# Kernel optimization log

Hardware: AMD Instinct MI355X
Metric: run time of the kernel (lower is better)

Reference implementation:

```python
import jax, jax.numpy as jnp
import numpy as np

N, D1, D2, B = 8, 2048, 1024, 512
D = D1 * D2
MAXBW = 3
NUM_PART = 5          # num_possible_partitions
TEMP = 0.01           # TEMPERATURE used in df_lt
DENOS = (3.0, 5.0, 17.0)  # 2^2-1, 2^2+1, 2^4+1


def ste_floor(x):
    # straight-through floor: forward floor, backward identity
    return x + jax.lax.stop_gradient(jnp.floor(x) - x)


def segmented_mean(piece, scheme, msp):
    """Replicates the inner python scan over sorted rows.
    piece:  (N, D) sorted residual errors
    scheme: (N-1, D) rounded split decisions (0/1), per column
    msp:    (N-1, D) soft split probabilities (grad factors), per column
    Returns (N, D): each row gets grad_ * (segment mean) of its segment.
    """
    n = piece.shape[0]
    buf = jnp.zeros_like(piece[0])
    cnt = jnp.zeros_like(piece[0])
    g = jnp.ones_like(piece[0])
    reset = jnp.zeros(piece.shape[1], dtype=bool)
    vlist, blist = [], []
    for i in range(n):
        buf = jnp.where(reset, piece[i], buf + piece[i])
        cnt = jnp.where(reset, 1.0, cnt + 1.0)
        g = jnp.where(reset, 1.0, g)
        if i == n - 1:
            vlist.append(g * (buf / cnt))
            blist.append(jnp.ones_like(reset))
        else:
            b = scheme[i] > 0.5
            vlist.append(jnp.where(b, g * msp[i], 0.0) * (buf / cnt))
            blist.append(b)
            g = jnp.where(b, g, g * (1.0 - msp[i]))
            reset = b
    # broadcast each segment-end value back to all rows of its segment
    out = vlist[-1]
    outs = [out]
    for i in range(n - 2, -1, -1):
        out = jnp.where(blist[i], vlist[i], out)
        outs.append(out)
    return jnp.stack(outs[::-1], axis=0)


def residual_quant(U, vsum, s, thr):
    """One residual quantization level (the update_partition=True branch)."""
    res = U - vsum                                   # (N, D)
    idx_maps = jnp.argsort(res, axis=0)              # torch.sort ascending, dim=0
    sorted_err = jnp.take_along_axis(res, idx_maps, axis=0)
    delta = sorted_err[1:] - sorted_err[:-1]         # (N-1, D), >= 0
    delta = delta / jnp.max(delta)
    msp = jax.nn.sigmoid((delta - thr) / TEMP)       # mean_split_point (N-1, D)
    rs = jnp.round(msp)                              # round_split, 0/1

    nm1 = N - 1
    P = 2 ** nm1  # all possible split-column patterns (torch.unique over dim=1)
    weights = (2 ** jnp.arange(nm1 - 1, -1, -1)).astype(jnp.int32)  # row 0 = MSB (lexicographic)
    code = jnp.sum(rs.astype(jnp.int32) * weights[:, None], axis=0)  # (D,)
    counts = jnp.zeros((P,), jnp.int32).at[code].add(1)
    present = counts > 0
    # torch.unique sorts patterns lexicographically -> rank = #present codes below
    rank_of_code = jnp.cumsum(present.astype(jnp.int32)) - present.astype(jnp.int32)
    order = jnp.argsort(-counts)                     # codes by count descending
    top_codes = order[:NUM_PART]
    top_ranks = rank_of_code[top_codes]              # s_indices[:NUM_PART]
    # binary patterns for every possible code
    patterns = ((jnp.arange(P)[:, None] >> jnp.arange(nm1 - 1, -1, -1)[None, :]) & 1).astype(jnp.float32)  # (P, N-1)
    inter = patterns @ patterns[top_codes].T         # (P, NUM_PART)
    sel = jnp.argmax(inter, axis=1)
    reassigned = top_ranks[sel]                      # (P,)
    is_top = jnp.any(rank_of_code[:, None] == top_ranks[None, :], axis=1)
    final_rank = jnp.where(is_top, rank_of_code, reassigned)  # (P,)
    c_rank = final_rank[code]                        # clustered_indices, (D,)

    # NOTE: original indexes round_split / mean_split_point columns BY the
    # unique-cluster index value s_idx (a quirk of the source); replicate it.
    scheme_used = rs[:, c_rank]                      # (N-1, D)
    msp_used = msp[:, c_rank]                        # (N-1, D)

    inner = segmented_mean(sorted_err, scheme_used, msp_used)  # (N, D)
    # einsum('cb,cba->ab', inner, one_hot(idx_maps)) == unsort along dim 0
    inv = jnp.argsort(idx_maps, axis=0)
    grouped = jnp.take_along_axis(inner, inv, axis=0)
    return s * ste_floor(grouped / s)


def setup_inputs():
    key = jax.random.key(0)
    k1, k2 = jax.random.split(key)
    x = jax.random.normal(k1, (B, N, D1), dtype=jnp.float32)
    # kaiming_normal_ on (N, D): std = sqrt(2 / fan_in), fan_in = D
    U = jax.random.normal(k2, (N, D), dtype=jnp.float32) * np.float32(np.sqrt(2.0 / D))
    thres_mean = jnp.full((D2,), -1.3, dtype=jnp.float32)
    return {"x": x, "U": U, "thres_mean": thres_mean}


def reference(x, U, thres_mean):
    beta = jnp.max(U)
    alpha = jnp.min(U)
    s = (beta - alpha) / DENOS[0]
    vsum = s * ste_floor(U / s)                      # base quantization level
    thr = jax.nn.sigmoid(jnp.repeat(thres_mean, D1))  # thres_mean.repeat_interleave(D1)
    for deno in DENOS[1:MAXBW]:
        s = s / deno
        vsum = vsum + residual_quant(U, vsum, s, thr)
    w = vsum.reshape(N, D1, D2)
    return jnp.einsum('bnd,ndl->bnl', x, w)
```

## Files before the change

### kernel.cpp

```cpp
#include <hip/hip_runtime.h>
#include <hip/hip_bf16.h>
#include <math.h>

#define NROW 8
#define DT   2097152
#define DD1  2048
#define DD2  1024
#define BATCH 512
#define NBLK4 2048


typedef __attribute__((ext_vector_type(8))) short short8;
typedef __attribute__((ext_vector_type(4))) float f32x4;

__device__ __forceinline__ unsigned fenc(float f){
  unsigned u = __float_as_uint(f);
  return (u & 0x80000000u) ? ~u : (u | 0x80000000u);
}
__device__ __forceinline__ float fdec(unsigned k){
  return (k & 0x80000000u) ? __uint_as_float(k ^ 0x80000000u) : __uint_as_float(~k);
}
__device__ __forceinline__ float sigmoid_ref(float z){
  #pragma clang fp contract(off)
  return 1.0f / (1.0f + expf(-z));
}
__device__ __forceinline__ unsigned short f2bf(float f){
  __hip_bfloat16 h = __float2bfloat16(f);
  return *reinterpret_cast<unsigned short*>(&h);
}
__device__ __forceinline__ float base1(float u, float s1, float inv_s1){
  #pragma clang fp contract(off)
  return s1 * floorf(u * inv_s1);
}
__device__ __forceinline__ void async16(const unsigned short* g, unsigned short* l){
  __builtin_amdgcn_global_load_lds((const __attribute__((address_space(1))) unsigned int*)g,
                                   (__attribute__((address_space(3))) unsigned int*)l, 16, 0, 0);
}

#define CSWAPV(a,b) { float _lo=fminf(a,b), _hi=fmaxf(a,b); a=_lo; b=_hi; }
__device__ __forceinline__ void sort8v(float v[8]){
  CSWAPV(v[0],v[1]) CSWAPV(v[2],v[3]) CSWAPV(v[4],v[5]) CSWAPV(v[6],v[7])
  CSWAPV(v[0],v[2]) CSWAPV(v[1],v[3]) CSWAPV(v[4],v[6]) CSWAPV(v[5],v[7])
  CSWAPV(v[1],v[2]) CSWAPV(v[5],v[6])
  CSWAPV(v[0],v[4]) CSWAPV(v[1],v[5]) CSWAPV(v[2],v[6]) CSWAPV(v[3],v[7])
  CSWAPV(v[2],v[4]) CSWAPV(v[3],v[5])
  CSWAPV(v[1],v[2]) CSWAPV(v[3],v[4]) CSWAPV(v[5],v[6])
}
__device__ __forceinline__ void cswapkv(float&av,int&ai,float&bv,int&bi){
  bool sw = (av > bv) || ((av == bv) && (ai > bi));
  float nav = sw ? bv : av; float nbv = sw ? av : bv;
  int   nai = sw ? bi : ai; int   nbi = sw ? ai : bi;
  av = nav; bv = nbv; ai = nai; bi = nbi;
}
#define CSWAPK(i,j) cswapkv(v[i],ix[i],v[j],ix[j]);
__device__ __forceinline__ void sort8kv(float v[8], int ix[8]){
  CSWAPK(0,1) CSWAPK(2,3) CSWAPK(4,5) CSWAPK(6,7)
  CSWAPK(0,2) CSWAPK(1,3) CSWAPK(4,6) CSWAPK(5,7)
  CSWAPK(1,2) CSWAPK(5,6)
  CSWAPK(0,4) CSWAPK(1,5) CSWAPK(2,6) CSWAPK(3,7)
  CSWAPK(2,4) CSWAPK(3,5)
  CSWAPK(1,2) CSWAPK(3,4) CSWAPK(5,6)
}

__global__ void k_init(unsigned* __restrict__ meta){
  int t = threadIdx.x;
  if (t == 0){ meta[0] = 0u; meta[1] = 0xFFFFFFFFu; meta[2] = 0u; meta[3] = 0u; }
  if (t < 128){ meta[4+t] = 0u; meta[132+t] = 0u; }
}

__global__ __launch_bounds__(256) void k_minmax(const float* __restrict__ U, unsigned* __restrict__ meta){
  __shared__ unsigned smx[256], smn[256];
  int t = threadIdx.x;
  size_t i = (size_t)blockIdx.x*256 + t;
  size_t stride = (size_t)gridDim.x*256;
  const float4* U4 = (const float4*)U;
  float mx = -INFINITY, mn = INFINITY;
  for (; i < (size_t)NROW*DT/4; i += stride){
    float4 v = U4[i];
    mx = fmaxf(fmaxf(mx,v.x), fmaxf(v.y, fmaxf(v.z,v.w)));
    mn = fminf(fminf(mn,v.x), fminf(v.y, fminf(v.z,v.w)));
  }
  smx[t] = fenc(mx); smn[t] = fenc(mn);
  __syncthreads();
  for (int o = 128; o > 0; o >>= 1){
    if (t < o){ smx[t] = max(smx[t], smx[t+o]); smn[t] = min(smn[t], smn[t+o]); }
    __syncthreads();
  }
  if (t == 0){ atomicMax(&meta[0], smx[0]); atomicMin(&meta[1], smn[0]); }
}

__global__ __launch_bounds__(256) void k_passA2(const float* __restrict__ U, unsigned* __restrict__ meta){
  #pragma clang fp contract(off)
  __shared__ unsigned sred[256];
  int t = threadIdx.x;
  int d0 = (blockIdx.x*256 + t)*4;
  float beta = fdec(meta[0]), alpha = fdec(meta[1]);
  float s1 = (beta - alpha) / 3.0f;
  float inv_s1 = 1.0f / s1;
  float4 u[8];
  #pragma unroll
  for (int i = 0; i < 8; ++i) u[i] = *(const float4*)(U + (size_t)i*DT + d0);
  unsigned dmax = 0u;
  #pragma unroll
  for (int c = 0; c < 4; ++c){
    float res[8];
    #pragma unroll
    for (int i = 0; i < 8; ++i){
      float uv = ((const float*)&u[i])[c];
      res[i] = uv - base1(uv, s1, inv_s1);
    }
    sort8v(res);
    float m = 0.0f;
    #pragma unroll
    for (int i = 0; i < 7; ++i) m = fmaxf(m, res[i+1] - res[i]);
    dmax = max(dmax, __float_as_uint(m));
  }
  sred[t] = dmax;
  __syncthreads();
  for (int o = 128; o > 0; o >>= 1){
    if (t < o) sred[t] = max(sred[t], sred[t+o]);
    __syncthreads();
  }
  if (t == 0) atomicMax(&meta[2], sred[0]);
}

template<int LEVEL>
__global__ __launch_bounds__(256) void k_passB(const float* __restrict__ U, const float* __restrict__ vsum,
                                               const float* __restrict__ thres_mean,
                                               unsigned char* __restrict__ code, unsigned* __restrict__ meta){
  #pragma clang fp contract(off)
  __shared__ int hist[128];
  int t = threadIdx.x;
  if (t < 128) hist[t] = 0;
  __syncthreads();
  int d0 = (blockIdx.x*256 + t)*4;
  float beta = fdec(meta[0]), alpha = fdec(meta[1]);
  float s1 = (beta - alpha) / 3.0f;
  float inv_s1 = 1.0f / s1;
  float gmax = __uint_as_float(meta[(LEVEL==2)?2:3]);
  float inv_gmax = 1.0f / gmax;
  float4 u[8], b[8];
  #pragma unroll
  for (int i = 0; i < 8; ++i){
    u[i] = *(const float4*)(U + (size_t)i*DT + d0);
    if (LEVEL == 2){
      float4 bb;
      bb.x = base1(u[i].x, s1, inv_s1); bb.y = base1(u[i].y, s1, inv_s1);
      bb.z = base1(u[i].z, s1, inv_s1); bb.w = base1(u[i].w, s1, inv_s1);
      b[i] = bb;
    } else {
      b[i] = *(const float4*)(vsum + (size_t)i*DT + d0);
    }
  }
  float thr = sigmoid_ref(thres_mean[d0 >> 11]);
  uchar4 cods;
  unsigned char* cp = (unsigned char*)&cods;
  #pragma unroll
  for (int c = 0; c < 4; ++c){
    float res[8];
    #pragma unroll
    for (int i = 0; i < 8; ++i) res[i] = ((const float*)&u[i])[c] - ((const float*)&b[i])[c];
    sort8v(res);
    int cd = 0;
    #pragma unroll
    for (int i = 0; i < 7; ++i){
      float dn = (res[i+1] - res[i]) * inv_gmax;
      int bit = (dn > thr) ? 1 : 0;
      cd = (cd << 1) | bit;
    }
    cp[c] = (unsigned char)cd;
    atomicAdd(&hist[cd], 1);
  }
  *(uchar4*)(code + d0) = cods;
  __syncthreads();
  if (t < 128 && hist[t] > 0) atomicAdd((int*)&meta[((LEVEL==2)?4:132) + t], hist[t]);
}

template<int LEVEL>
__global__ void k_small(const float* __restrict__ U, const float* __restrict__ vsum,
                        const float* __restrict__ thres_mean, unsigned* __restrict__ meta){
  #pragma clang fp contract(off)
  __shared__ int cs[128], rk[128], redk[128];
  __shared__ int top_code[5], top_rank[5];
  __shared__ int w0cnt;
  int c = threadIdx.x;
  cs[c] = (int)meta[((LEVEL==2)?4:132) + c];
  bool present = cs[c] > 0;
  unsigned long long bm = __ballot(present);
  int lane = c & 63;
  int r = (int)__popcll(bm & ((1ull << lane) - 1ull));
  if (c == 63) w0cnt = (int)__popcll(bm);
  __syncthreads();
  if (c >= 64) r += w0cnt;
  rk[c] = r;
  __syncthreads();
  for (int k = 0; k < 5; ++k){
    redk[c] = (cs[c] << 7) | (127 - c);
    __syncthreads();
    for (int o = 64; o > 0; o >>= 1){
      if (c < o) redk[c] = max(redk[c], redk[c+o]);
      __syncthreads();
    }
    if (c == 0){
      int best = 127 - (redk[0] & 127);
      top_code[k] = best; top_rank[k] = rk[best];
      cs[best] = -1;
    }
    __syncthreads();
  }
  int besti = -1, sel = 0;
  #pragma unroll
  for (int j = 0; j < 5; ++j){
    int inter = __popc(c & top_code[j]);
    if (inter > besti){ besti = inter; sel = j; }
  }
  bool is_top = false;
  #pragma unroll
  for (int j = 0; j < 5; ++j) is_top = is_top || (rk[c] == top_rank[j]);
  int fr = is_top ? rk[c] : top_rank[sel];
  ((int*)meta)[260 + c] = fr;
  float beta = fdec(meta[0]), alpha = fdec(meta[1]);
  float s1 = (beta - alpha) / 3.0f;
  float inv_s1 = 1.0f / s1;
  float gmax = __uint_as_float(meta[(LEVEL==2)?2:3]);
  float res[8];
  #pragma unroll
  for (int i = 0; i < 8; ++i){
    size_t off = (size_t)i*DT + c;
    float u = U[off];
    float b = (LEVEL==2) ? base1(u, s1, inv_s1) : vsum[off];
    res[i] = u - b;
  }
  sort8v(res);
  float thr = sigmoid_ref(thres_mean[c >> 11]);
  unsigned bits = 0;
  float* msp_tab = (float*)&meta[388];
  #pragma unroll
  for (int i = 0; i < 7; ++i){
    float dn  = (res[i+1] - res[i]) / gmax;
    float z   = (dn - thr) / 0.01f;
    float msp = sigmoid_ref(z);
    msp_tab[c*7 + i] = msp;
    bits |= ((unsigned)(int)rintf(msp)) << i;
  }
  meta[1284 + c] = bits;
}

template<int LEVEL>
__global__ __launch_bounds__(256) void k_passD(const float* __restrict__ U, float* __restrict__ vsum,
                                               const unsigned char* __restrict__ code,
                                               unsigned* __restrict__ meta){
  #pragma clang fp contract(off)
  __shared__ float q_lds[32*256];
  __shared__ int fr_s[128];
  __shared__ unsigned bits_s[128];
  __shared__ float msp_s[128*7];
  __shared__ unsigned sred[256];
  int t = threadIdx.x;
  if (t < 128){ fr_s[t] = ((int*)meta)[260 + t]; bits_s[t] = meta[1284 + t]; }
  for (int i = t; i < 128*7; i += 256) msp_s[i] = ((float*)&meta[388])[i];
  __syncthreads();
  int d0 = (blockIdx.x*256 + t)*4;
  float beta = fdec(meta[0]), alpha = fdec(meta[1]);
  float s1 = (beta - alpha) / 3.0f;
  float inv_s1 = 1.0f / s1;
  float s2 = s1 / 5.0f;
  float s  = (LEVEL == 2) ? s2 : (s2 / 17.0f);
  float inv_s = 1.0f / s;
  float4 u4[8], b4[8];
  #pragma unroll
  for (int i = 0; i < 8; ++i){
    u4[i] = *(const float4*)(U + (size_t)i*DT + d0);
    if (LEVEL == 2){
      float4 bb;
      bb.x = base1(u4[i].x, s1, inv_s1); bb.y = base1(u4[i].y, s1, inv_s1);
      bb.z = base1(u4[i].z, s1, inv_s1); bb.w = base1(u4[i].w, s1, inv_s1);
      b4[i] = bb;
    } else {
      b4[i] = *(const float4*)(vsum + (size_t)i*DT + d0);
    }
  }
  uchar4 cods = *(const uchar4*)(code + d0);
  const unsigned char* cp = (const unsigned char*)&cods;
  #pragma unroll
  for (int c = 0; c < 4; ++c){
    float v[8]; int ix[8];
    #pragma unroll
    for (int i = 0; i < 8; ++i){
      v[i] = ((const float*)&u4[i])[c] - ((const float*)&b4[i])[c];
      ix[i] = i;
    }
    sort8kv(v, ix);
    int cr = fr_s[cp[c]];
    unsigned sb = bits_s[cr];
    float vv[8]; bool bl[8];
    float buf = 0.0f, cnt = 0.0f, g = 1.0f; bool reset = false;
    #pragma unroll
    for (int i = 0; i < 8; ++i){
      buf = reset ? v[i] : (buf + v[i]);
      cnt = reset ? 1.0f : (cnt + 1.0f);
      g   = reset ? 1.0f : g;
      float m = buf * __builtin_amdgcn_rcpf(cnt);
      if (i == 7){ vv[7] = g * m; bl[7] = true; }
      else {
        float msp = msp_s[cr*7 + i];
        bool b = ((sb >> i) & 1u) != 0u;
        vv[i] = b ? ((g * msp) * m) : 0.0f;
        bl[i] = b;
        g = b ? g : (g * (1.0f - msp));
        reset = b;
      }
    }
    float out = vv[7];
    float inner[8];
    inner[7] = out;
    for (int i = 6; i >= 0; --i){ if (bl[i]) out = vv[i]; inner[i] = out; }
    #pragma unroll
    for (int i = 0; i < 8; ++i){
      float q = s * floorf(inner[i] * inv_s);
      q_lds[(ix[i]*4 + c)*256 + t] = q;
    }
  }
  float4 vn4[8];
  unsigned dmax = 0u;
  #pragma unroll
  for (int c = 0; c < 4; ++c){
    float res3[8];
    #pragma unroll
    for (int rr = 0; rr < 8; ++rr){
      float q = q_lds[(rr*4 + c)*256 + t];
      float vn = ((const float*)&b4[rr])[c] + q;
      ((float*)&vn4[rr])[c] = vn;
      if (LEVEL == 2) res3[rr] = ((const float*)&u4[rr])[c] - vn;
    }
    if (LEVEL == 2){
      sort8v(res3);
      float m = 0.0f;
      #pragma unroll
      for (int i = 0; i < 7; ++i) m = fmaxf(m, res3[i+1] - res3[i]);
      dmax = max(dmax, __float_as_uint(m));
    }
  }
  #pragma unroll
  for (int rr = 0; rr < 8; ++rr)
    *(float4*)(vsum + (size_t)rr*DT + d0) = vn4[rr];
  if (LEVEL == 2){
    sred[t] = dmax;
    __syncthreads();
    for (int o = 128; o > 0; o >>= 1){
      if (t < o) sred[t] = max(sred[t], sred[t+o]);
      __syncthreads();
    }
    if (t == 0) atomicMax(&meta[3], sred[0]);
  }
}

__global__ __launch_bounds__(256) void k_wt(const float* __restrict__ vsum, unsigned short* __restrict__ wt){
  __shared__ unsigned short tile[64][68];
  int t = threadIdx.x;
  int c4 = t & 15, r0 = t >> 4;
  int n = blockIdx.z, k0 = blockIdx.y*64, l0 = blockIdx.x*64;
  const float* src = vsum + (size_t)n*DT;
  #pragma unroll
  for (int i = 0; i < 4; ++i){
    int r = r0 + i*16;
    float4 v = *(const float4*)(src + (size_t)(k0+r)*DD2 + l0 + c4*4);
    tile[r][c4*4+0] = f2bf(v.x); tile[r][c4*4+1] = f2bf(v.y);
    tile[r][c4*4+2] = f2bf(v.z); tile[r][c4*4+3] = f2bf(v.w);
  }
  __syncthreads();
  unsigned short* dst = wt + (size_t)n*DT;
  #pragma unroll
  for (int i = 0; i < 4; ++i){
    int rl = r0 + i*16;
    ushort4 o;
    o.x = tile[c4*4+0][rl]; o.y = tile[c4*4+1][rl];
    o.z = tile[c4*4+2][rl]; o.w = tile[c4*4+3][rl];
    *(ushort4*)(dst + (size_t)(l0+rl)*DD1 + k0 + c4*4) = o;
  }
}

__global__ __launch_bounds__(256) void k_xb(const float* __restrict__ x, unsigned short* __restrict__ xb){
  int idx = (blockIdx.x*256 + threadIdx.x)*4;
  float4 v = *(const float4*)(x + idx);
  ushort4 o;
  o.x = f2bf(v.x); o.y = f2bf(v.y); o.z = f2bf(v.z); o.w = f2bf(v.w);
  *(ushort4*)(xb + idx) = o;
}

__global__ __launch_bounds__(256) void k_gemm(const unsigned short* __restrict__ xb,
                                              const unsigned short* __restrict__ wt,
                                              float* __restrict__ out){
  __shared__ __align__(16) unsigned short As[64*64];
  __shared__ __align__(16) unsigned short Bs[128*64];
  int t = threadIdx.x;
  int lane = t & 63, wv = t >> 6;
  int n  = blockIdx.z;
  int b0 = blockIdx.y * 64;
  int l0 = blockIdx.x * 128;
  int wm = (wv >> 1) * 32, wn = (wv & 1) * 64;
  int col = lane & 15, quad = lane >> 4;
  int arow = lane >> 3, aseg = lane & 7;
  const unsigned short* wtn = wt + (size_t)n*DT;
  f32x4 acc[2][4] = {};
  for (int k0 = 0; k0 < DD1; k0 += 64){
    #pragma unroll
    for (int i = 0; i < 2; ++i){
      int row = wv*16 + i*8 + arow;
      const unsigned short* g = xb + (((size_t)(b0+row)*NROW + n)*DD1 + k0 + aseg*8);
      async16(g, &As[(wv*16 + i*8)*64]);
    }
    #pragma unroll
    for (int i = 0; i < 4; ++i){
      int row = wv*32 + i*8 + arow;
      const unsigned short* g = wtn + ((size_t)(l0+row)*DD1 + k0 + aseg*8);
      async16(g, &Bs[(wv*32 + i*8)*64]);
    }
    __syncthreads();
    #pragma unroll
    for (int ks = 0; ks < 2; ++ks){
      int kq = ks*32 + quad*8;
      short8 af[2], bfr[4];
      #pragma unroll
      for (int mi = 0; mi < 2; ++mi) af[mi]  = *(const short8*)&As[(wm + mi*16 + col)*64 + kq];
      #pragma unroll
      for (int ni = 0; ni < 4; ++ni) bfr[ni] = *(const short8*)&Bs[(wn + ni*16 + col)*64 + kq];
      #pragma unroll
      for (int mi = 0; mi < 2; ++mi)
        #pragma unroll
        for (int ni = 0; ni < 4; ++ni)
          acc[mi][ni] = __builtin_amdgcn_mfma_f32_16x16x32_bf16(af[mi], bfr[ni], acc[mi][ni], 0, 0, 0);
    }
    __syncthreads();
  }
  #pragma unroll
  for (int mi = 0; mi < 2; ++mi)
    #pragma unroll
    for (int ni = 0; ni < 4; ++ni)
      #pragma unroll
      for (int r = 0; r < 4; ++r){
        int b = b0 + wm + mi*16 + quad*4 + r;
        int l = l0 + wn + ni*16 + col;
        out[((size_t)b*NROW + n)*DD2 + l] = acc[mi][ni][r];
      }
}

extern "C" void kernel_launch(void* const* d_in, const int* in_sizes, int n_in,
                              void* d_out, int out_size, void* d_ws, size_t ws_size,
                              hipStream_t stream){
  const float* x  = (const float*)d_in[0];
  const float* U  = (const float*)d_in[1];
  const float* tm = (const float*)d_in[2];
  float* out  = (float*)d_out;
  float* vsum = (float*)d_ws;
  unsigned char* code = (unsigned char*)d_ws + (size_t)NROW*DT*4;
  unsigned short* wt  = (unsigned short*)((unsigned char*)d_ws + (size_t)NROW*DT*4 + DT);
  unsigned* meta = (unsigned*)((unsigned char*)d_ws + (size_t)NROW*DT*4 + DT + (size_t)NROW*DT*2);
  unsigned short* xb = (unsigned short*)d_ws;
  (void)in_sizes; (void)n_in; (void)out_size; (void)ws_size;

  k_init  <<<1,    256, 0, stream>>>(meta);
  k_minmax<<<2048, 256, 0, stream>>>(U, meta);

  k_passA2  <<<NBLK4, 256, 0, stream>>>(U, meta);
  k_passB<2><<<NBLK4, 256, 0, stream>>>(U, vsum, tm, code, meta);
  k_small<2><<<1,    128, 0, stream>>>(U, vsum, tm, meta);
  k_passD<2><<<NBLK4, 256, 0, stream>>>(U, vsum, code, meta);

  k_passB<3><<<NBLK4, 256, 0, stream>>>(U, vsum, tm, code, meta);
  k_small<3><<<1,    128, 0, stream>>>(U, vsum, tm, meta);
  k_passD<3><<<NBLK4, 256, 0, stream>>>(U, vsum, code, meta);

  k_wt  <<<dim3(DD2/64, DD1/64, NROW), 256, 0, stream>>>(vsum, wt);
  k_xb  <<<(BATCH*NROW*DD1)/1024, 256, 0, stream>>>(x, xb);
  k_gemm<<<dim3(DD2/128, BATCH/64, NROW), 256, 0, stream>>>(xb, wt, out);
}
```

Measured before the change: 428.7 us.

## Fuse quantization passes into one cooperative persistent kernel with grid syncs

Replaces the chain of init, min/max, passA, passB, small and passD launches with a single cooperative kernel. The kernel uses grid-wide syncs and per-block slot arrays for the global reductions in place of atomics and separate launches. The aim is to cut launch gaps and small serial kernels between the memory-bound passes. The cost is grid.sync overhead, a grid capped at 1024 blocks that may reduce memory parallelism, and serial small phases that leave the rest of the grid idle while block 0 works.

```diff
diff --git a/kernel.cpp b/kernel.cpp
--- a/kernel.cpp
+++ b/kernel.cpp
@@ -1,13 +1,16 @@
 #include <hip/hip_runtime.h>
 #include <hip/hip_bf16.h>
+#include <hip/hip_cooperative_groups.h>
 #include <math.h>
+
+namespace cg = cooperative_groups;
 
 #define NROW 8
 #define DT   2097152
 #define DD1  2048
 #define DD2  1024
 #define BATCH 512
-#define NBLK4 2048
+#define NGRP 2048
 
 
 typedef __attribute__((ext_vector_type(8))) short short8;
@@ -62,83 +65,13 @@
   CSWAPK(1,2) CSWAPK(3,4) CSWAPK(5,6)
 }
 
-__global__ void k_init(unsigned* __restrict__ meta){
-  int t = threadIdx.x;
-  if (t == 0){ meta[0] = 0u; meta[1] = 0xFFFFFFFFu; meta[2] = 0u; meta[3] = 0u; }
-  if (t < 128){ meta[4+t] = 0u; meta[132+t] = 0u; }
-}
-
-__global__ __launch_bounds__(256) void k_minmax(const float* __restrict__ U, unsigned* __restrict__ meta){
-  __shared__ unsigned smx[256], smn[256];
-  int t = threadIdx.x;
-  size_t i = (size_t)blockIdx.x*256 + t;
-  size_t stride = (size_t)gridDim.x*256;
-  const float4* U4 = (const float4*)U;
-  float mx = -INFINITY, mn = INFINITY;
-  for (; i < (size_t)NROW*DT/4; i += stride){
-    float4 v = U4[i];
-    mx = fmaxf(fmaxf(mx,v.x), fmaxf(v.y, fmaxf(v.z,v.w)));
-    mn = fminf(fminf(mn,v.x), fminf(v.y, fminf(v.z,v.w)));
-  }
-  smx[t] = fenc(mx); smn[t] = fenc(mn);
-  __syncthreads();
-  for (int o = 128; o > 0; o >>= 1){
-    if (t < o){ smx[t] = max(smx[t], smx[t+o]); smn[t] = min(smn[t], smn[t+o]); }
-    __syncthreads();
-  }
-  if (t == 0){ atomicMax(&meta[0], smx[0]); atomicMin(&meta[1], smn[0]); }
-}
-
-__global__ __launch_bounds__(256) void k_passA2(const float* __restrict__ U, unsigned* __restrict__ meta){
+
+template<int LEVEL>
+__device__ __forceinline__ void passB_group(
+    int d0, const float* __restrict__ U, const float* __restrict__ vsum,
+    const float* __restrict__ tm, float s1, float inv_s1, float inv_gmax,
+    unsigned char* __restrict__ code, int* hist){
   #pragma clang fp contract(off)
-  __shared__ unsigned sred[256];
-  int t = threadIdx.x;
-  int d0 = (blockIdx.x*256 + t)*4;
-  float beta = fdec(meta[0]), alpha = fdec(meta[1]);
-  float s1 = (beta - alpha) / 3.0f;
-  float inv_s1 = 1.0f / s1;
-  float4 u[8];
-  #pragma unroll
-  for (int i = 0; i < 8; ++i) u[i] = *(const float4*)(U + (size_t)i*DT + d0);
-  unsigned dmax = 0u;
-  #pragma unroll
-  for (int c = 0; c < 4; ++c){
-    float res[8];
-    #pragma unroll
-    for (int i = 0; i < 8; ++i){
-      float uv = ((const float*)&u[i])[c];
-      res[i] = uv - base1(uv, s1, inv_s1);
-    }
-    sort8v(res);
-    float m = 0.0f;
-    #pragma unroll
-    for (int i = 0; i < 7; ++i) m = fmaxf(m, res[i+1] - res[i]);
-    dmax = max(dmax, __float_as_uint(m));
-  }
-  sred[t] = dmax;
-  __syncthreads();
-  for (int o = 128; o > 0; o >>= 1){
-    if (t < o) sred[t] = max(sred[t], sred[t+o]);
-    __syncthreads();
-  }
-  if (t == 0) atomicMax(&meta[2], sred[0]);
-}
-
-template<int LEVEL>
-__global__ __launch_bounds__(256) void k_passB(const float* __restrict__ U, const float* __restrict__ vsum,
-                                               const float* __restrict__ thres_mean,
-                                               unsigned char* __restrict__ code, unsigned* __restrict__ meta){
-  #pragma clang fp contract(off)
-  __shared__ int hist[128];
-  int t = threadIdx.x;
-  if (t < 128) hist[t] = 0;
-  __syncthreads();
-  int d0 = (blockIdx.x*256 + t)*4;
-  float beta = fdec(meta[0]), alpha = fdec(meta[1]);
-  float s1 = (beta - alpha) / 3.0f;
-  float inv_s1 = 1.0f / s1;
-  float gmax = __uint_as_float(meta[(LEVEL==2)?2:3]);
-  float inv_gmax = 1.0f / gmax;
   float4 u[8], b[8];
   #pragma unroll
   for (int i = 0; i < 8; ++i){
@@ -152,7 +85,7 @@
       b[i] = *(const float4*)(vsum + (size_t)i*DT + d0);
     }
   }
-  float thr = sigmoid_ref(thres_mean[d0 >> 11]);
+  float thr = sigmoid_ref(tm[d0 >> 11]);
   uchar4 cods;
   unsigned char* cp = (unsigned char*)&cods;
   #pragma unroll
@@ -165,108 +98,21 @@
     #pragma unroll
     for (int i = 0; i < 7; ++i){
       float dn = (res[i+1] - res[i]) * inv_gmax;
-      int bit = (dn > thr) ? 1 : 0;
-      cd = (cd << 1) | bit;
+      cd = (cd << 1) | ((dn > thr) ? 1 : 0);
     }
     cp[c] = (unsigned char)cd;
     atomicAdd(&hist[cd], 1);
   }
   *(uchar4*)(code + d0) = cods;
-  __syncthreads();
-  if (t < 128 && hist[t] > 0) atomicAdd((int*)&meta[((LEVEL==2)?4:132) + t], hist[t]);
 }
 
 template<int LEVEL>
-__global__ void k_small(const float* __restrict__ U, const float* __restrict__ vsum,
-                        const float* __restrict__ thres_mean, unsigned* __restrict__ meta){
+__device__ __forceinline__ unsigned passD_group(
+    int d0, int t, const float* __restrict__ U, float* __restrict__ vsum,
+    const unsigned char* __restrict__ code,
+    float s1, float inv_s1, float s, float inv_s,
+    const int* fr_s, const unsigned* bits_s, const float* msp_s, float* q_lds){
   #pragma clang fp contract(off)
-  __shared__ int cs[128], rk[128], redk[128];
-  __shared__ int top_code[5], top_rank[5];
-  __shared__ int w0cnt;
-  int c = threadIdx.x;
-  cs[c] = (int)meta[((LEVEL==2)?4:132) + c];
-  bool present = cs[c] > 0;
-  unsigned long long bm = __ballot(present);
-  int lane = c & 63;
-  int r = (int)__popcll(bm & ((1ull << lane) - 1ull));
-  if (c == 63) w0cnt = (int)__popcll(bm);
-  __syncthreads();
-  if (c >= 64) r += w0cnt;
-  rk[c] = r;
-  __syncthreads();
-  for (int k = 0; k < 5; ++k){
-    redk[c] = (cs[c] << 7) | (127 - c);
-    __syncthreads();
-    for (int o = 64; o > 0; o >>= 1){
-      if (c < o) redk[c] = max(redk[c], redk[c+o]);
-      __syncthreads();
-    }
-    if (c == 0){
-      int best = 127 - (redk[0] & 127);
-      top_code[k] = best; top_rank[k] = rk[best];
-      cs[best] = -1;
-    }
-    __syncthreads();
-  }
-  int besti = -1, sel = 0;
-  #pragma unroll
-  for (int j = 0; j < 5; ++j){
-    int inter = __popc(c & top_code[j]);
-    if (inter > besti){ besti = inter; sel = j; }
-  }
-  bool is_top = false;
-  #pragma unroll
-  for (int j = 0; j < 5; ++j) is_top = is_top || (rk[c] == top_rank[j]);
-  int fr = is_top ? rk[c] : top_rank[sel];
-  ((int*)meta)[260 + c] = fr;
-  float beta = fdec(meta[0]), alpha = fdec(meta[1]);
-  float s1 = (beta - alpha) / 3.0f;
-  float inv_s1 = 1.0f / s1;
-  float gmax = __uint_as_float(meta[(LEVEL==2)?2:3]);
-  float res[8];
-  #pragma unroll
-  for (int i = 0; i < 8; ++i){
-    size_t off = (size_t)i*DT + c;
-    float u = U[off];
-    float b = (LEVEL==2) ? base1(u, s1, inv_s1) : vsum[off];
-    res[i] = u - b;
-  }
-  sort8v(res);
-  float thr = sigmoid_ref(thres_mean[c >> 11]);
-  unsigned bits = 0;
-  float* msp_tab = (float*)&meta[388];
-  #pragma unroll
-  for (int i = 0; i < 7; ++i){
-    float dn  = (res[i+1] - res[i]) / gmax;
-    float z   = (dn - thr) / 0.01f;
-    float msp = sigmoid_ref(z);
-    msp_tab[c*7 + i] = msp;
-    bits |= ((unsigned)(int)rintf(msp)) << i;
-  }
-  meta[1284 + c] = bits;
-}
-
-template<int LEVEL>
-__global__ __launch_bounds__(256) void k_passD(const float* __restrict__ U, float* __restrict__ vsum,
-                                               const unsigned char* __restrict__ code,
-                                               unsigned* __restrict__ meta){
-  #pragma clang fp contract(off)
-  __shared__ float q_lds[32*256];
-  __shared__ int fr_s[128];
-  __shared__ unsigned bits_s[128];
-  __shared__ float msp_s[128*7];
-  __shared__ unsigned sred[256];
-  int t = threadIdx.x;
-  if (t < 128){ fr_s[t] = ((int*)meta)[260 + t]; bits_s[t] = meta[1284 + t]; }
-  for (int i = t; i < 128*7; i += 256) msp_s[i] = ((float*)&meta[388])[i];
-  __syncthreads();
-  int d0 = (blockIdx.x*256 + t)*4;
-  float beta = fdec(meta[0]), alpha = fdec(meta[1]);
-  float s1 = (beta - alpha) / 3.0f;
-  float inv_s1 = 1.0f / s1;
-  float s2 = s1 / 5.0f;
-  float s  = (LEVEL == 2) ? s2 : (s2 / 17.0f);
-  float inv_s = 1.0f / s;
   float4 u4[8], b4[8];
   #pragma unroll
   for (int i = 0; i < 8; ++i){
@@ -344,15 +190,234 @@
   #pragma unroll
   for (int rr = 0; rr < 8; ++rr)
     *(float4*)(vsum + (size_t)rr*DT + d0) = vn4[rr];
-  if (LEVEL == 2){
-    sred[t] = dmax;
+  return dmax;
+}
+
+template<int LEVEL>
+__device__ void small_phase(const float* __restrict__ U, const float* __restrict__ vsum,
+                            const float* __restrict__ tm, unsigned* __restrict__ meta,
+                            float s1, float inv_s1, float gmax, float* q_lds){
+  #pragma clang fp contract(off)
+  int c = threadIdx.x;
+  int* cs   = (int*)q_lds;
+  int* rk   = cs + 128;
+  int* redk = rk + 128;
+  int* tc   = redk + 128;
+  int* tr   = tc + 8;
+  int* w0c  = tr + 8;
+  if (c < 128) cs[c] = (int)meta[((LEVEL==2)?4:132) + c];
+  __syncthreads();
+  if (c < 128){
+    bool present = cs[c] > 0;
+    unsigned long long bm = __ballot(present);
+    int lane = c & 63;
+    rk[c] = (int)__popcll(bm & ((1ull << lane) - 1ull));
+    if (c == 63) *w0c = (int)__popcll(bm);
+  }
+  __syncthreads();
+  if (c >= 64 && c < 128) rk[c] += *w0c;
+  __syncthreads();
+  for (int k = 0; k < 5; ++k){
+    if (c < 128) redk[c] = (cs[c] << 7) | (127 - c);
+    __syncthreads();
+    for (int o = 64; o > 0; o >>= 1){
+      if (c < o) redk[c] = max(redk[c], redk[c+o]);
+      __syncthreads();
+    }
+    if (c == 0){
+      int best = 127 - (redk[0] & 127);
+      tc[k] = best; tr[k] = rk[best];
+      cs[best] = -1;
+    }
+    __syncthreads();
+  }
+  if (c < 128){
+    int besti = -1, sel = 0;
+    #pragma unroll
+    for (int j = 0; j < 5; ++j){
+      int inter = __popc(c & tc[j]);
+      if (inter > besti){ besti = inter; sel = j; }
+    }
+    bool is_top = false;
+    #pragma unroll
+    for (int j = 0; j < 5; ++j) is_top = is_top || (rk[c] == tr[j]);
+    ((int*)meta)[260 + c] = is_top ? rk[c] : tr[sel];
+    float res[8];
+    #pragma unroll
+    for (int i = 0; i < 8; ++i){
+      size_t off = (size_t)i*DT + c;
+      float u = U[off];
+      float b = (LEVEL==2) ? base1(u, s1, inv_s1) : vsum[off];
+      res[i] = u - b;
+    }
+    sort8v(res);
+    float thr = sigmoid_ref(tm[c >> 11]);
+    unsigned bits = 0;
+    float* msp_tab = (float*)(meta + 388);
+    #pragma unroll
+    for (int i = 0; i < 7; ++i){
+      float dn  = (res[i+1] - res[i]) / gmax;
+      float z   = (dn - thr) / 0.01f;
+      float msp = sigmoid_ref(z);
+      msp_tab[c*7 + i] = msp;
+      bits |= ((unsigned)(int)rintf(msp)) << i;
+    }
+    meta[1284 + c] = bits;
+  }
+  __syncthreads();
+}
+
+__global__ void __launch_bounds__(256, 4) k_quant(
+    const float* __restrict__ U, const float* __restrict__ tm,
+    float* __restrict__ vsum, unsigned char* __restrict__ code,
+    unsigned* __restrict__ meta, unsigned* __restrict__ slots){
+  #pragma clang fp contract(off)
+  cg::grid_group grid = cg::this_grid();
+  int t = threadIdx.x, b = blockIdx.x, nb = gridDim.x;
+
+  __shared__ __align__(16) float q_lds[32*256];
+  __shared__ int fr_s[128];
+  __shared__ unsigned bits_s[128];
+  __shared__ float msp_s[896];
+  __shared__ unsigned redA[256], redB[256];
+
+  if (b == 0 && t < 128){ meta[4+t] = 0u; meta[132+t] = 0u; }
+  float mx = -INFINITY, mn = INFINITY;
+  for (int grp = b; grp < NGRP; grp += nb){
+    int d0 = grp*1024 + t*4;
+    #pragma unroll
+    for (int i = 0; i < 8; ++i){
+      float4 v = *(const float4*)(U + (size_t)i*DT + d0);
+      mx = fmaxf(mx, fmaxf(fmaxf(v.x,v.y), fmaxf(v.z,v.w)));
+      mn = fminf(mn, fminf(fminf(v.x,v.y), fminf(v.z,v.w)));
+    }
+  }
+  redA[t] = fenc(mx); redB[t] = fenc(mn);
+  __syncthreads();
+  for (int o = 128; o > 0; o >>= 1){
+    if (t < o){ redA[t] = max(redA[t], redA[t+o]); redB[t] = min(redB[t], redB[t+o]); }
+    __syncthreads();
+  }
+  if (t == 0){ slots[b] = redA[0]; slots[2048 + b] = redB[0]; }
+  grid.sync();
+  {
+    unsigned vx = 0u, vn = 0xFFFFFFFFu;
+    for (int i = t; i < nb; i += 256){ vx = max(vx, slots[i]); vn = min(vn, slots[2048+i]); }
+    __syncthreads();
+    redA[t] = vx; redB[t] = vn;
     __syncthreads();
     for (int o = 128; o > 0; o >>= 1){
-      if (t < o) sred[t] = max(sred[t], sred[t+o]);
+      if (t < o){ redA[t] = max(redA[t], redA[t+o]); redB[t] = min(redB[t], redB[t+o]); }
       __syncthreads();
     }
-    if (t == 0) atomicMax(&meta[3], sred[0]);
-  }
+  }
+  float beta = fdec(redA[0]), alpha = fdec(redB[0]);
+  __syncthreads();
+  float s1 = (beta - alpha) / 3.0f;
+  float inv_s1 = 1.0f / s1;
+  float s2 = s1 / 5.0f, s3 = s2 / 17.0f;
+  float inv_s2 = 1.0f / s2, inv_s3 = 1.0f / s3;
+
+  unsigned dmax = 0u;
+  for (int grp = b; grp < NGRP; grp += nb){
+    int d0 = grp*1024 + t*4;
+    float4 u[8];
+    #pragma unroll
+    for (int i = 0; i < 8; ++i) u[i] = *(const float4*)(U + (size_t)i*DT + d0);
+    #pragma unroll
+    for (int c = 0; c < 4; ++c){
+      float res[8];
+      #pragma unroll
+      for (int i = 0; i < 8; ++i){
+        float uv = ((const float*)&u[i])[c];
+        res[i] = uv - base1(uv, s1, inv_s1);
+      }
+      sort8v(res);
+      float m = 0.0f;
+      #pragma unroll
+      for (int i = 0; i < 7; ++i) m = fmaxf(m, res[i+1] - res[i]);
+      dmax = max(dmax, __float_as_uint(m));
+    }
+  }
+  redA[t] = dmax;
+  __syncthreads();
+  for (int o = 128; o > 0; o >>= 1){
+    if (t < o) redA[t] = max(redA[t], redA[t+o]);
+    __syncthreads();
+  }
+  if (t == 0) slots[4096 + b] = redA[0];
+  grid.sync();
+  {
+    unsigned vx = 0u;
+    for (int i = t; i < nb; i += 256) vx = max(vx, slots[4096+i]);
+    __syncthreads();
+    redA[t] = vx;
+    __syncthreads();
+    for (int o = 128; o > 0; o >>= 1){
+      if (t < o) redA[t] = max(redA[t], redA[t+o]);
+      __syncthreads();
+    }
+  }
+  float gmax2 = __uint_as_float(redA[0]);
+  __syncthreads();
+  float inv_gmax2 = 1.0f / gmax2;
+
+  int* hist = (int*)q_lds;
+  if (t < 128) hist[t] = 0;
+  __syncthreads();
+  for (int grp = b; grp < NGRP; grp += nb)
+    passB_group<2>(grp*1024 + t*4, U, vsum, tm, s1, inv_s1, inv_gmax2, code, hist);
+  __syncthreads();
+  if (t < 128){ int h = hist[t]; if (h) atomicAdd((int*)&meta[4+t], h); }
+  grid.sync();
+  if (b == 0) small_phase<2>(U, vsum, tm, meta, s1, inv_s1, gmax2, q_lds);
+  grid.sync();
+  if (t < 128){ fr_s[t] = ((const int*)meta)[260+t]; bits_s[t] = meta[1284+t]; }
+  for (int i = t; i < 896; i += 256) msp_s[i] = ((const float*)(meta+388))[i];
+  __syncthreads();
+  unsigned dmax3 = 0u;
+  for (int grp = b; grp < NGRP; grp += nb)
+    dmax3 = max(dmax3, passD_group<2>(grp*1024 + t*4, t, U, vsum, code,
+                                      s1, inv_s1, s2, inv_s2, fr_s, bits_s, msp_s, q_lds));
+  __syncthreads();
+  redA[t] = dmax3;
+  __syncthreads();
+  for (int o = 128; o > 0; o >>= 1){
+    if (t < o) redA[t] = max(redA[t], redA[t+o]);
+    __syncthreads();
+  }
+  if (t == 0) slots[4096 + b] = redA[0];
+  grid.sync();
+  {
+    unsigned vx = 0u;
+    for (int i = t; i < nb; i += 256) vx = max(vx, slots[4096+i]);
+    __syncthreads();
+    redA[t] = vx;
+    __syncthreads();
+    for (int o = 128; o > 0; o >>= 1){
+      if (t < o) redA[t] = max(redA[t], redA[t+o]);
+      __syncthreads();
+    }
+  }
+  float gmax3 = __uint_as_float(redA[0]);
+  __syncthreads();
+  float inv_gmax3 = 1.0f / gmax3;
+
+  if (t < 128) hist[t] = 0;
+  __syncthreads();
+  for (int grp = b; grp < NGRP; grp += nb)
+    passB_group<3>(grp*1024 + t*4, U, vsum, tm, s1, inv_s1, inv_gmax3, code, hist);
+  __syncthreads();
+  if (t < 128){ int h = hist[t]; if (h) atomicAdd((int*)&meta[132+t], h); }
+  grid.sync();
+  if (b == 0) small_phase<3>(U, vsum, tm, meta, s1, inv_s1, gmax3, q_lds);
+  grid.sync();
+  if (t < 128){ fr_s[t] = ((const int*)meta)[260+t]; bits_s[t] = meta[1284+t]; }
+  for (int i = t; i < 896; i += 256) msp_s[i] = ((const float*)(meta+388))[i];
+  __syncthreads();
+  for (int grp = b; grp < NGRP; grp += nb)
+    passD_group<3>(grp*1024 + t*4, t, U, vsum, code,
+                   s1, inv_s1, s3, inv_s3, fr_s, bits_s, msp_s, q_lds);
 }
 
 __global__ __launch_bounds__(256) void k_wt(const float* __restrict__ vsum, unsigned short* __restrict__ wt){
@@ -439,9 +504,9 @@
     for (int ni = 0; ni < 4; ++ni)
       #pragma unroll
       for (int r = 0; r < 4; ++r){
-        int b = b0 + wm + mi*16 + quad*4 + r;
+        int bb = b0 + wm + mi*16 + quad*4 + r;
         int l = l0 + wn + ni*16 + col;
-        out[((size_t)b*NROW + n)*DD2 + l] = acc[mi][ni][r];
+        out[((size_t)bb*NROW + n)*DD2 + l] = acc[mi][ni][r];
       }
 }
 
@@ -453,23 +518,22 @@
   const float* tm = (const float*)d_in[2];
   float* out  = (float*)d_out;
   float* vsum = (float*)d_ws;
-  unsigned char* code = (unsigned char*)d_ws + (size_t)NROW*DT*4;
-  unsigned short* wt  = (unsigned short*)((unsigned char*)d_ws + (size_t)NROW*DT*4 + DT);
-  unsigned* meta = (unsigned*)((unsigned char*)d_ws + (size_t)NROW*DT*4 + DT + (size_t)NROW*DT*2);
+  unsigned char* code = (unsigned char*)d_ws + 67108864;
+  unsigned short* wt  = (unsigned short*)((unsigned char*)d_ws + 69206016);
+  unsigned* meta  = (unsigned*)((unsigned char*)d_ws + 102760448);
+  unsigned* slots = (unsigned*)((unsigned char*)d_ws + 102768640);
   unsigned short* xb = (unsigned short*)d_ws;
   (void)in_sizes; (void)n_in; (void)out_size; (void)ws_size;
 
-  k_init  <<<1,    256, 0, stream>>>(meta);
-  k_minmax<<<2048, 256, 0, stream>>>(U, meta);
-
-  k_passA2  <<<NBLK4, 256, 0, stream>>>(U, meta);
-  k_passB<2><<<NBLK4, 256, 0, stream>>>(U, vsum, tm, code, meta);
-  k_small<2><<<1,    128, 0, stream>>>(U, vsum, tm, meta);
-  k_passD<2><<<NBLK4, 256, 0, stream>>>(U, vsum, code, meta);
-
-  k_passB<3><<<NBLK4, 256, 0, stream>>>(U, vsum, tm, code, meta);
-  k_small<3><<<1,    128, 0, stream>>>(U, vsum, tm, meta);
-  k_passD<3><<<NBLK4, 256, 0, stream>>>(U, vsum, code, meta);
+  int mb = 0;
+  hipOccupancyMaxActiveBlocksPerMultiprocessor(&mb, k_quant, 256, 0);
+  int grid = mb * 256;
+  if (grid > 1024) grid = 1024;
+  if (grid < 1)    grid = 256;
+  const float* U_ = U; const float* tm_ = tm;
+  float* vs_ = vsum; unsigned char* cd_ = code; unsigned* mt_ = meta; unsigned* sl_ = slots;
+  void* args[] = { (void*)&U_, (void*)&tm_, (void*)&vs_, (void*)&cd_, (void*)&mt_, (void*)&sl_ };
+  hipLaunchCooperativeKernel((void*)k_quant, dim3(grid), dim3(256), args, 0, stream);
 
   k_wt  <<<dim3(DD2/64, DD1/64, NROW), 256, 0, stream>>>(vsum, wt);
   k_xb  <<<(BATCH*NROW*DD1)/1024, 256, 0, stream>>>(x, xb);
```

Result: slower. 695.4 us (+62.2%).
